# Optimization experiments

Measured on AMD Instinct MI355X. Metric: run time of the kernel, lower is better.

Reference implementation:

```python
import jax, jax.numpy as jnp
import numpy as np

DIM = 768
HEADS = 12
HEAD_DIM = DIM // HEADS
SCALE = HEAD_DIM ** -0.5


def setup_inputs() -> dict:
    key = jax.random.key(0)
    ks = jax.random.split(key, 7)
    B, N, C = 4, 1024, DIM
    s = 0.02
    return {
        "x": jax.random.normal(ks[0], (B, N, C), dtype=jnp.float32),
        "attn_mask": jax.random.normal(ks[1], (B, N, N), dtype=jnp.float32) * 0.1,
        "w_qkv": jax.random.normal(ks[2], (3 * C, C), dtype=jnp.float32) * s,
        "w_proj": jax.random.normal(ks[3], (C, C), dtype=jnp.float32) * s,
        "b_proj": jnp.zeros((C,), dtype=jnp.float32),
        "w_pre": jax.random.normal(ks[4], (HEADS, HEADS), dtype=jnp.float32) * 0.2,
        "w_post": jax.random.normal(ks[5], (HEADS, HEADS), dtype=jnp.float32) * 0.2,
    }


def reference(x, attn_mask, w_qkv, w_proj, b_proj, w_pre, w_post):
    B, N, C = x.shape
    H, D = HEADS, HEAD_DIM
    qkv = (x @ w_qkv.T).reshape(B, N, 3, H, D)
    q, k, v = jnp.moveaxis(qkv, 2, 0)          # each [B, N, H, D]
    q = q.transpose(0, 2, 1, 3)                # [B, H, N, D]
    k = k.transpose(0, 2, 1, 3)
    v = v.transpose(0, 2, 1, 3)
    attn = jnp.einsum("bhnd,bhmd->bhnm", q, k) * SCALE
    attn = attn + attn_mask[:, None, :, :]
    # talking-heads pre-softmax mixing: Linear over head axis (y = x @ W.T)
    attn = jnp.einsum("bhnm,gh->bgnm", attn, w_pre)
    attn = jax.nn.softmax(attn, axis=-1)
    # talking-heads post-softmax mixing
    attn = jnp.einsum("bhnm,gh->bgnm", attn, w_post)
    out = jnp.einsum("bhnm,bhmd->bhnd", attn, v)   # [B, H, N, D]
    out = out.transpose(0, 2, 1, 3).reshape(B, N, C)
    return out @ w_proj.T + b_proj
```

## Files before the change

kernel.cpp:

```cpp
#include <hip/hip_runtime.h>
#include <hip/hip_bf16.h>

typedef __attribute__((ext_vector_type(8))) short bf16x8;
typedef __attribute__((ext_vector_type(8))) short s16x8;
typedef __attribute__((ext_vector_type(4))) float f32x4;
typedef __attribute__((ext_vector_type(2))) float f32x2;
typedef unsigned short u16;
typedef unsigned int u32;

__device__ __forceinline__ u16 f2bf(float f){
  __hip_bfloat16 h = __float2bfloat16(f);
  return *reinterpret_cast<u16*>(&h);
}
__device__ __forceinline__ float bflo(u32 w){ return __uint_as_float(w << 16); }
__device__ __forceinline__ float bfhi(u32 w){ return __uint_as_float(w & 0xffff0000u); }

__device__ __forceinline__ void gload_lds16(const u16* g, u16* l){
  __builtin_amdgcn_global_load_lds(
      (__attribute__((address_space(1))) u32*)g,
      (__attribute__((address_space(3))) u32*)l, 16, 0, 0);
}

__global__ __launch_bounds__(256) void cvt3_kernel(
    const float* __restrict__ s0, u16* __restrict__ d0, int n0,
    const float* __restrict__ s1, u16* __restrict__ d1, int n1,
    const float* __restrict__ s2, u16* __restrict__ d2, int n2)
{
  int i = blockIdx.x*256 + threadIdx.x;
  const float* s; u16* d; int idx; float sc = 1.f;
  if (i < n0){ s = s0; d = d0; idx = i; }
  else if (i < n0 + n1){
    idx = i - n0; s = s1; d = d1;
    if (idx < 768*192) sc = 0.125f;
  } else if (i < n0 + n1 + n2){
    idx = i - n0 - n1; s = s2; d = d2;
  } else return;
  float4 v = reinterpret_cast<const float4*>(s)[idx];
  ushort4 o;
  o.x = f2bf(v.x*sc); o.y = f2bf(v.y*sc); o.z = f2bf(v.z*sc); o.w = f2bf(v.w*sc);
  reinterpret_cast<ushort4*>(d)[idx] = o;
}

template<int BM, int BN, int MODE>
__global__ __launch_bounds__(256) void gemm_bt(
    const u16* __restrict__ A, const u16* __restrict__ B,
    void* __restrict__ C0, void* __restrict__ C1, void* __restrict__ C2,
    const float* __restrict__ bias,
    int M, int N, int K, int lda, int ldb, long sA, long sB, long sC)
{
  constexpr int BK = 32, LDT = 32;
  __shared__ __align__(16) u16 As[BM*LDT];
  __shared__ __align__(16) u16 Bs[BN*LDT];
  const int z = blockIdx.z;
  const u16* Ab = A + (long)z * sA;
  const u16* Bb = B + (long)z * sB;
  const int bm = blockIdx.x * BM, bn = blockIdx.y * BN;
  const int tid = threadIdx.x, lane = tid & 63, wv = tid >> 6;
  constexpr int WM = BM/2, WN = BN/2, FM = WM/16, FN = WN/16;
  const int wm = (wv >> 1) * WM, wn = (wv & 1) * WN;
  const int quad = lane >> 4, cl = lane & 15;
  f32x4 acc[FM][FN];
  #pragma unroll
  for (int i=0;i<FM;i++)
    #pragma unroll
    for (int j=0;j<FN;j++){ f32x4 zr = {0.f,0.f,0.f,0.f}; acc[i][j] = zr; }
  constexpr int AIT = (BM*BK)/(8*256);
  constexpr int BIT = (BN*BK)/(8*256);

  for (int kb = 0; kb < K; kb += BK){
    __syncthreads();
    #pragma unroll
    for (int sL=0; sL<AIT; sL++){
      int e = tid + sL*256, r = e >> 2, c8 = (e & 3) * 8;
      gload_lds16(Ab + (long)(bm + r)*lda + kb + c8, &As[e*8]);
    }
    #pragma unroll
    for (int sL=0; sL<BIT; sL++){
      int e = tid + sL*256, r = e >> 2, c8 = (e & 3) * 8;
      gload_lds16(Bb + (long)(bn + r)*ldb + kb + c8, &Bs[e*8]);
    }
    __syncthreads();
    bf16x8 af[FM], bfr[FN];
    #pragma unroll
    for (int i=0;i<FM;i++)
      af[i] = *reinterpret_cast<const bf16x8*>(&As[(wm + i*16 + cl)*LDT + quad*8]);
    #pragma unroll
    for (int j=0;j<FN;j++)
      bfr[j] = *reinterpret_cast<const bf16x8*>(&Bs[(wn + j*16 + cl)*LDT + quad*8]);
    #pragma unroll
    for (int i=0;i<FM;i++)
      #pragma unroll
      for (int j=0;j<FN;j++)
        acc[i][j] = __builtin_amdgcn_mfma_f32_16x16x32_bf16(af[i], bfr[j], acc[i][j], 0, 0, 0);
  }

  #pragma unroll
  for (int i=0;i<FM;i++)
  #pragma unroll
  for (int j=0;j<FN;j++)
  #pragma unroll
  for (int r=0;r<4;r++){
    int gm = bm + wm + i*16 + quad*4 + r;
    int gn = bn + wn + j*16 + cl;
    float v = acc[i][j][r];
    if (MODE == 0){
      int b_ = gm >> 10, n_ = gm & 1023;
      int t3 = (gn >= 1536) ? 2 : ((gn >= 768) ? 1 : 0);
      int rem = gn - t3*768;
      int h = rem >> 6, d = rem & 63;
      u16 hv = f2bf(v);
      if (t3 == 0)      ((u16*)C0)[((long)((b_*12 + h)*1024 + n_))*64 + d] = hv;
      else if (t3 == 1) ((u16*)C1)[((long)((b_*12 + h)*1024 + n_))*64 + d] = hv;
      else              ((u16*)C2)[((long)((b_*12 + h)*64 + d))*1024 + n_] = hv;
    } else if (MODE == 1){
      ((u16*)C0)[(long)z*sC + (long)gm*N + gn] = f2bf(v);
    } else if (MODE == 2){
      int b_ = z / 12, h = z - b_*12;
      ((u16*)C0)[((long)((b_*1024 + gm)*12 + h))*64 + gn] = f2bf(v);
    } else {
      ((float*)C0)[(long)gm*N + gn] = v + bias[gn];
    }
  }
}

__global__ __launch_bounds__(256) void mix_kernel(
    u16* __restrict__ S, const float* __restrict__ mask,
    const float* __restrict__ w_pre, const float* __restrict__ w_post)
{
  const int bid = blockIdx.x;
  const int b = bid >> 10, n = bid & 1023;
  const int t = threadIdx.x;
  const int wv = t >> 6, lane = t & 63;
  const int m0 = t * 4;
  const long base0 = (((long)(b*12))*1024 + n) * 1024;

  uint2 raw[12];
  #pragma unroll
  for (int h=0; h<12; h++)
    raw[h] = *reinterpret_cast<const uint2*>(S + base0 + (long)h*1024*1024 + m0);
  float4 mk4 = *reinterpret_cast<const float4*>(mask + ((long)(b*1024 + n))*1024 + m0);

  f32x2 smix[12][2];
  {
    f32x2 mkA = {mk4.x, mk4.y}, mkB = {mk4.z, mk4.w};
    #pragma unroll
    for (int g=0; g<12; g++){
      float rs = 0.f;
      #pragma unroll
      for (int h=0; h<12; h++) rs += w_pre[g*12 + h];
      smix[g][0] = rs * mkA;
      smix[g][1] = rs * mkB;
    }
  }
  #pragma unroll
  for (int h=0; h<12; h++){
    f32x2 s0 = {bflo(raw[h].x), bfhi(raw[h].x)};
    f32x2 s1 = {bflo(raw[h].y), bfhi(raw[h].y)};
    #pragma unroll
    for (int g=0; g<12; g++){
      float w = w_pre[g*12 + h];
      smix[g][0] += w * s0;
      smix[g][1] += w * s1;
    }
  }

  __shared__ float redM[12][4];
  __shared__ float redS[12][4];
  float M[12];
  #pragma unroll
  for (int g=0; g<12; g++)
    M[g] = fmaxf(fmaxf(smix[g][0][0], smix[g][0][1]),
                 fmaxf(smix[g][1][0], smix[g][1][1]));
  #pragma unroll
  for (int off=32; off>0; off>>=1)
    #pragma unroll
    for (int g=0; g<12; g++) M[g] = fmaxf(M[g], __shfl_xor(M[g], off));
  if (lane == 0){
    #pragma unroll
    for (int g=0; g<12; g++) redM[g][wv] = M[g];
  }
  __syncthreads();
  #pragma unroll
  for (int g=0; g<12; g++)
    M[g] = fmaxf(fmaxf(redM[g][0], redM[g][1]), fmaxf(redM[g][2], redM[g][3]));

  float L[12];
  #pragma unroll
  for (int g=0; g<12; g++){
    smix[g][0] -= M[g];
    smix[g][1] -= M[g];
    float e0 = __expf(smix[g][0][0]);
    float e1 = __expf(smix[g][0][1]);
    float e2 = __expf(smix[g][1][0]);
    float e3 = __expf(smix[g][1][1]);
    smix[g][0][0]=e0; smix[g][0][1]=e1; smix[g][1][0]=e2; smix[g][1][1]=e3;
    L[g] = (e0 + e1) + (e2 + e3);
  }
  #pragma unroll
  for (int off=32; off>0; off>>=1)
    #pragma unroll
    for (int g=0; g<12; g++) L[g] += __shfl_xor(L[g], off);
  if (lane == 0){
    #pragma unroll
    for (int g=0; g<12; g++) redS[g][wv] = L[g];
  }
  __syncthreads();
  #pragma unroll
  for (int g=0; g<12; g++){
    float Lt = (redS[g][0] + redS[g][1]) + (redS[g][2] + redS[g][3]);
    float inv;
    asm("v_rcp_f32 %0, %1" : "=v"(inv) : "v"(Lt));
    smix[g][0] *= inv;
    smix[g][1] *= inv;
  }

  #pragma unroll
  for (int h=0; h<12; h++){
    f32x2 o0, o1;
    {
      float w = w_post[h*12];
      o0 = w * smix[0][0];
      o1 = w * smix[0][1];
    }
    #pragma unroll
    for (int g=1; g<12; g++){
      float w = w_post[h*12 + g];
      o0 += w * smix[g][0];
      o1 += w * smix[g][1];
    }
    ushort4 st;
    st.x = f2bf(o0[0]); st.y = f2bf(o0[1]);
    st.z = f2bf(o1[0]); st.w = f2bf(o1[1]);
    *reinterpret_cast<ushort4*>(S + base0 + (long)h*1024*1024 + m0) = st;
  }
}

extern "C" void kernel_launch(void* const* d_in, const int* in_sizes, int n_in,
                              void* d_out, int out_size, void* d_ws, size_t ws_size,
                              hipStream_t stream)
{
  const float* x      = (const float*)d_in[0];
  const float* mask   = (const float*)d_in[1];
  const float* w_qkv  = (const float*)d_in[2];
  const float* w_proj = (const float*)d_in[3];
  const float* b_proj = (const float*)d_in[4];
  const float* w_pre  = (const float*)d_in[5];
  const float* w_post = (const float*)d_in[6];
  float* out = (float*)d_out;

  u16* xb     = (u16*)d_ws;
  u16* wqkvb  = xb     + 4096l*768;
  u16* wprojb = wqkvb  + 2304l*768;
  u16* Qb     = wprojb + 768l*768;
  u16* Kb     = Qb     + 48l*1024*64;
  u16* Vtb    = Kb     + 48l*1024*64;
  u16* tmpb   = Vtb    + 48l*1024*64;
  u16* Sb     = tmpb   + 4096l*768;
  size_t need = ((size_t)(Sb - xb) + 48ul*1024*1024) * sizeof(u16);
  if (ws_size < need) return;

  const int n0 = 4096*768/4, n1 = 2304*768/4, n2 = 768*768/4;
  cvt3_kernel<<<(n0+n1+n2 + 255)/256, 256, 0, stream>>>(x, xb, n0, w_qkv, wqkvb, n1,
                                                        w_proj, wprojb, n2);

  dim3 gq(4096/128, 2304/128, 1);
  gemm_bt<128,128,0><<<gq, 256, 0, stream>>>(xb, wqkvb, Qb, Kb, Vtb, nullptr,
      4096, 2304, 768, 768, 768, 0, 0, 0);

  dim3 gs(1024/128, 1024/128, 48);
  gemm_bt<128,128,1><<<gs, 256, 0, stream>>>(Qb, Kb, Sb, nullptr, nullptr, nullptr,
      1024, 1024, 64, 64, 64, 1024l*64, 1024l*64, 1024l*1024);

  mix_kernel<<<4096, 256, 0, stream>>>(Sb, mask, w_pre, w_post);

  dim3 gp(1024/64, 1, 48);
  gemm_bt<64,64,2><<<gp, 256, 0, stream>>>(Sb, Vtb, tmpb, nullptr, nullptr, nullptr,
      1024, 64, 1024, 1024, 1024, 1024l*1024, 64l*1024, 0);

  dim3 go(4096/128, 768/128, 1);
  gemm_bt<128,128,3><<<go, 256, 0, stream>>>(tmpb, wprojb, out, nullptr, nullptr, b_proj,
      4096, 768, 768, 768, 768, 0, 0, 0);
}
```

Before: 248.4 us.

## Fuse talking-heads mixing and softmax into the attention-times-V MFMA kernel

```diff
diff --git a/kernel.cpp b/kernel.cpp
--- a/kernel.cpp
+++ b/kernel.cpp
@@ -2,9 +2,9 @@
 #include <hip/hip_bf16.h>
 
 typedef __attribute__((ext_vector_type(8))) short bf16x8;
-typedef __attribute__((ext_vector_type(8))) short s16x8;
 typedef __attribute__((ext_vector_type(4))) float f32x4;
 typedef __attribute__((ext_vector_type(2))) float f32x2;
+typedef __attribute__((ext_vector_type(4))) unsigned int u32x4;
 typedef unsigned short u16;
 typedef unsigned int u32;
 
@@ -14,6 +14,9 @@
 }
 __device__ __forceinline__ float bflo(u32 w){ return __uint_as_float(w << 16); }
 __device__ __forceinline__ float bfhi(u32 w){ return __uint_as_float(w & 0xffff0000u); }
+__device__ __forceinline__ u32 pack2bf(float a, float b){
+  return (u32)f2bf(a) | ((u32)f2bf(b) << 16);
+}
 
 __device__ __forceinline__ void gload_lds16(const u16* g, u16* l){
   __builtin_amdgcn_global_load_lds(
@@ -114,124 +117,202 @@
       else              ((u16*)C2)[((long)((b_*12 + h)*64 + d))*1024 + n_] = hv;
     } else if (MODE == 1){
       ((u16*)C0)[(long)z*sC + (long)gm*N + gn] = f2bf(v);
-    } else if (MODE == 2){
-      int b_ = z / 12, h = z - b_*12;
-      ((u16*)C0)[((long)((b_*1024 + gm)*12 + h))*64 + gn] = f2bf(v);
     } else {
       ((float*)C0)[(long)gm*N + gn] = v + bias[gn];
     }
   }
 }
 
-__global__ __launch_bounds__(256) void mix_kernel(
-    u16* __restrict__ S, const float* __restrict__ mask,
-    const float* __restrict__ w_pre, const float* __restrict__ w_post)
+__global__ __launch_bounds__(512, 2) void fused_mixpv(
+    const u16* __restrict__ S, const u16* __restrict__ Vt,
+    const float* __restrict__ mask,
+    const float* __restrict__ w_pre, const float* __restrict__ w_post,
+    u16* __restrict__ tmp)
 {
-  const int bid = blockIdx.x;
-  const int b = bid >> 10, n = bid & 1023;
-  const int t = threadIdx.x;
-  const int wv = t >> 6, lane = t & 63;
-  const int m0 = t * 4;
-  const long base0 = (((long)(b*12))*1024 + n) * 1024;
-
-  uint2 raw[12];
-  #pragma unroll
-  for (int h=0; h<12; h++)
-    raw[h] = *reinterpret_cast<const uint2*>(S + base0 + (long)h*1024*1024 + m0);
-  float4 mk4 = *reinterpret_cast<const float4*>(mask + ((long)(b*1024 + n))*1024 + m0);
-
-  f32x2 smix[12][2];
+  const int b  = blockIdx.y;
+  const int n0 = blockIdx.x * 16;
+  const int t  = threadIdx.x;
+  const int w  = t >> 6, lane = t & 63;
+  const int quad = lane >> 4, cl = lane & 15;
+  const int n = n0 + cl;
+
+  __shared__ float Lp[8][12][16];
+  __shared__ float invL[12][16];
+  __shared__ float O_lds[12][16][65];
+
+  const long srow = ((long)(b*12)*1024 + n) * 1024;
+  const float* mrow = mask + ((long)(b*1024 + n))*1024;
+
+  float rsv[12];
+  #pragma unroll
+  for (int g=0; g<12; g++){
+    float a = 0.f;
+    #pragma unroll
+    for (int h=0; h<12; h++) a += w_pre[g*12 + h];
+    rsv[g] = a;
+  }
+
+  float L1[12];
+  #pragma unroll
+  for (int g=0; g<12; g++) L1[g] = 0.f;
+
+  for (int ts=0; ts<4; ts++){
+    int mb = w*128 + ts*32 + quad*8;
+    float4 k0 = *reinterpret_cast<const float4*>(mrow + mb);
+    float4 k1 = *reinterpret_cast<const float4*>(mrow + mb + 4);
+    f32x2 mk[4] = {{k0.x,k0.y},{k0.z,k0.w},{k1.x,k1.y},{k1.z,k1.w}};
+    f32x2 sm[12][4];
+    #pragma unroll
+    for (int g=0; g<12; g++)
+      #pragma unroll
+      for (int p=0; p<4; p++) sm[g][p] = rsv[g] * mk[p];
+    #pragma unroll
+    for (int h=0; h<12; h++){
+      uint4 rw = *reinterpret_cast<const uint4*>(S + srow + (long)h*1048576 + mb);
+      f32x2 sv[4] = {{bflo(rw.x),bfhi(rw.x)},{bflo(rw.y),bfhi(rw.y)},
+                     {bflo(rw.z),bfhi(rw.z)},{bflo(rw.w),bfhi(rw.w)}};
+      #pragma unroll
+      for (int g=0; g<12; g++){
+        float wv = w_pre[g*12 + h];
+        #pragma unroll
+        for (int p=0; p<4; p++) sm[g][p] += wv * sv[p];
+      }
+    }
+    #pragma unroll
+    for (int g=0; g<12; g++){
+      float s0 = __expf(sm[g][0][0]) + __expf(sm[g][0][1]);
+      float s1 = __expf(sm[g][1][0]) + __expf(sm[g][1][1]);
+      float s2 = __expf(sm[g][2][0]) + __expf(sm[g][2][1]);
+      float s3 = __expf(sm[g][3][0]) + __expf(sm[g][3][1]);
+      L1[g] += (s0 + s1) + (s2 + s3);
+    }
+  }
+  #pragma unroll
+  for (int g=0; g<12; g++){
+    L1[g] += __shfl_xor(L1[g], 16);
+    L1[g] += __shfl_xor(L1[g], 32);
+  }
+  if (lane < 16){
+    #pragma unroll
+    for (int g=0; g<12; g++) Lp[w][g][lane] = L1[g];
+  }
+  __syncthreads();
+  if (t < 192){
+    int g = t >> 4, nn = t & 15;
+    float s = 0.f;
+    #pragma unroll
+    for (int w8=0; w8<8; w8++) s += Lp[w8][g][nn];
+    invL[g][nn] = 1.f / s;
+  }
+  __syncthreads();
+
+  const int mq = w & 3, hg = w >> 2;
+  float iLr[12];
+  #pragma unroll
+  for (int g=0; g<12; g++) iLr[g] = invL[g][cl];
+
+  f32x4 acc[6][4];
+  #pragma unroll
+  for (int i=0;i<6;i++)
+    #pragma unroll
+    for (int j=0;j<4;j++){ f32x4 zr = {0.f,0.f,0.f,0.f}; acc[i][j] = zr; }
+
+  const u16* vtb = Vt + (long)(b*12)*64*1024;
+
+  for (int st=0; st<8; st++){
+    const int ms = mq*256 + st*32;
+    const int mb = ms + quad*8;
+    u32 pa[6][4];
+    #pragma unroll
+    for (int sub=0; sub<2; sub++){
+      const int mbs = mb + sub*4;
+      float4 k4 = *reinterpret_cast<const float4*>(mrow + mbs);
+      f32x2 mkA = {k4.x, k4.y}, mkB = {k4.z, k4.w};
+      f32x2 sm[12][2];
+      #pragma unroll
+      for (int g=0; g<12; g++){ sm[g][0] = rsv[g]*mkA; sm[g][1] = rsv[g]*mkB; }
+      #pragma unroll
+      for (int h=0; h<12; h++){
+        uint2 rw = *reinterpret_cast<const uint2*>(S + srow + (long)h*1048576 + mbs);
+        f32x2 s0 = {bflo(rw.x), bfhi(rw.x)};
+        f32x2 s1 = {bflo(rw.y), bfhi(rw.y)};
+        #pragma unroll
+        for (int g=0; g<12; g++){
+          float wv = w_pre[g*12 + h];
+          sm[g][0] += wv * s0;
+          sm[g][1] += wv * s1;
+        }
+      }
+      #pragma unroll
+      for (int g=0; g<12; g++){
+        sm[g][0][0] = __expf(sm[g][0][0]) * iLr[g];
+        sm[g][0][1] = __expf(sm[g][0][1]) * iLr[g];
+        sm[g][1][0] = __expf(sm[g][1][0]) * iLr[g];
+        sm[g][1][1] = __expf(sm[g][1][1]) * iLr[g];
+      }
+      #pragma unroll
+      for (int h6=0; h6<6; h6++){
+        const int h = hg*6 + h6;
+        f32x2 o0, o1;
+        {
+          float wv = w_post[h*12];
+          o0 = wv * sm[0][0]; o1 = wv * sm[0][1];
+        }
+        #pragma unroll
+        for (int g=1; g<12; g++){
+          float wv = w_post[h*12 + g];
+          o0 += wv * sm[g][0];
+          o1 += wv * sm[g][1];
+        }
+        pa[h6][sub*2]     = pack2bf(o0[0], o0[1]);
+        pa[h6][sub*2 + 1] = pack2bf(o1[0], o1[1]);
+      }
+    }
+    #pragma unroll
+    for (int h6=0; h6<6; h6++){
+      const int h = hg*6 + h6;
+      union { u32x4 u; bf16x8 v; } fc;
+      fc.u = (u32x4){pa[h6][0], pa[h6][1], pa[h6][2], pa[h6][3]};
+      const u16* vp = vtb + ((long)h*64 + cl)*1024 + ms + quad*8;
+      #pragma unroll
+      for (int dj=0; dj<4; dj++){
+        bf16x8 bf = *reinterpret_cast<const bf16x8*>(vp + dj*16*1024);
+        acc[h6][dj] = __builtin_amdgcn_mfma_f32_16x16x32_bf16(fc.v, bf, acc[h6][dj], 0, 0, 0);
+      }
+    }
+  }
+
+  for (int r=0; r<4; r++){
+    if (mq == r){
+      #pragma unroll
+      for (int h6=0; h6<6; h6++)
+        #pragma unroll
+        for (int dj=0; dj<4; dj++)
+          #pragma unroll
+          for (int rr=0; rr<4; rr++){
+            float* p = &O_lds[hg*6 + h6][quad*4 + rr][dj*16 + cl];
+            if (r == 0) *p = acc[h6][dj][rr];
+            else        *p += acc[h6][dj][rr];
+          }
+    }
+    __syncthreads();
+  }
+
   {
-    f32x2 mkA = {mk4.x, mk4.y}, mkB = {mk4.z, mk4.w};
-    #pragma unroll
-    for (int g=0; g<12; g++){
-      float rs = 0.f;
-      #pragma unroll
-      for (int h=0; h<12; h++) rs += w_pre[g*12 + h];
-      smix[g][0] = rs * mkA;
-      smix[g][1] = rs * mkB;
-    }
-  }
-  #pragma unroll
-  for (int h=0; h<12; h++){
-    f32x2 s0 = {bflo(raw[h].x), bfhi(raw[h].x)};
-    f32x2 s1 = {bflo(raw[h].y), bfhi(raw[h].y)};
-    #pragma unroll
-    for (int g=0; g<12; g++){
-      float w = w_pre[g*12 + h];
-      smix[g][0] += w * s0;
-      smix[g][1] += w * s1;
-    }
-  }
-
-  __shared__ float redM[12][4];
-  __shared__ float redS[12][4];
-  float M[12];
-  #pragma unroll
-  for (int g=0; g<12; g++)
-    M[g] = fmaxf(fmaxf(smix[g][0][0], smix[g][0][1]),
-                 fmaxf(smix[g][1][0], smix[g][1][1]));
-  #pragma unroll
-  for (int off=32; off>0; off>>=1)
-    #pragma unroll
-    for (int g=0; g<12; g++) M[g] = fmaxf(M[g], __shfl_xor(M[g], off));
-  if (lane == 0){
-    #pragma unroll
-    for (int g=0; g<12; g++) redM[g][wv] = M[g];
-  }
-  __syncthreads();
-  #pragma unroll
-  for (int g=0; g<12; g++)
-    M[g] = fmaxf(fmaxf(redM[g][0], redM[g][1]), fmaxf(redM[g][2], redM[g][3]));
-
-  float L[12];
-  #pragma unroll
-  for (int g=0; g<12; g++){
-    smix[g][0] -= M[g];
-    smix[g][1] -= M[g];
-    float e0 = __expf(smix[g][0][0]);
-    float e1 = __expf(smix[g][0][1]);
-    float e2 = __expf(smix[g][1][0]);
-    float e3 = __expf(smix[g][1][1]);
-    smix[g][0][0]=e0; smix[g][0][1]=e1; smix[g][1][0]=e2; smix[g][1][1]=e3;
-    L[g] = (e0 + e1) + (e2 + e3);
-  }
-  #pragma unroll
-  for (int off=32; off>0; off>>=1)
-    #pragma unroll
-    for (int g=0; g<12; g++) L[g] += __shfl_xor(L[g], off);
-  if (lane == 0){
-    #pragma unroll
-    for (int g=0; g<12; g++) redS[g][wv] = L[g];
-  }
-  __syncthreads();
-  #pragma unroll
-  for (int g=0; g<12; g++){
-    float Lt = (redS[g][0] + redS[g][1]) + (redS[g][2] + redS[g][3]);
-    float inv;
-    asm("v_rcp_f32 %0, %1" : "=v"(inv) : "v"(Lt));
-    smix[g][0] *= inv;
-    smix[g][1] *= inv;
-  }
-
-  #pragma unroll
-  for (int h=0; h<12; h++){
-    f32x2 o0, o1;
-    {
-      float w = w_post[h*12];
-      o0 = w * smix[0][0];
-      o1 = w * smix[0][1];
-    }
-    #pragma unroll
-    for (int g=1; g<12; g++){
-      float w = w_post[h*12 + g];
-      o0 += w * smix[g][0];
-      o1 += w * smix[g][1];
-    }
-    ushort4 st;
-    st.x = f2bf(o0[0]); st.y = f2bf(o0[1]);
-    st.z = f2bf(o1[0]); st.w = f2bf(o1[1]);
-    *reinterpret_cast<ushort4*>(S + base0 + (long)h*1024*1024 + m0) = st;
+    const int nr = t >> 5, c0 = (t & 31) * 24;
+    u32 ow[12];
+    #pragma unroll
+    for (int e=0; e<24; e+=2){
+      int l0 = c0 + e,  h0 = l0 >> 6, d0 = l0 & 63;
+      int l1 = l0 + 1,  h1 = l1 >> 6, d1 = l1 & 63;
+      ow[e>>1] = pack2bf(O_lds[h0][nr][d0], O_lds[h1][nr][d1]);
+    }
+    u16* op = tmp + ((long)(b*1024 + n0 + nr))*768 + c0;
+    #pragma unroll
+    for (int q=0; q<3; q++){
+      u32x4 v4 = {ow[q*4], ow[q*4+1], ow[q*4+2], ow[q*4+3]};
+      *reinterpret_cast<u32x4*>(op + q*8) = v4;
+    }
   }
 }
 
@@ -271,11 +352,7 @@
   gemm_bt<128,128,1><<<gs, 256, 0, stream>>>(Qb, Kb, Sb, nullptr, nullptr, nullptr,
       1024, 1024, 64, 64, 64, 1024l*64, 1024l*64, 1024l*1024);
 
-  mix_kernel<<<4096, 256, 0, stream>>>(Sb, mask, w_pre, w_post);
-
-  dim3 gp(1024/64, 1, 48);
-  gemm_bt<64,64,2><<<gp, 256, 0, stream>>>(Sb, Vtb, tmpb, nullptr, nullptr, nullptr,
-      1024, 64, 1024, 1024, 1024, 1024l*1024, 64l*1024, 0);
+  fused_mixpv<<<dim3(64, 4), 512, 0, stream>>>(Sb, Vtb, mask, w_pre, w_post, tmpb);
 
   dim3 go(4096/128, 768/128, 1);
   gemm_bt<128,128,3><<<go, 256, 0, stream>>>(tmpb, wprojb, out, nullptr, nullptr, b_proj,
```

Result: slower. 758.2 us (+205.2%).
